# Optimization experiments

Measured on AMD Instinct MI355X. Metric: run time of the kernel, lower is better.

The kernel has to match this reference:

```python
import jax, jax.numpy as jnp
import numpy as np

C, H, R, INTER = 1024, 16, 16, 2816  # hidden, heads, lora rank, mlp intermediate
B, N = 2, 2048
EPS = 1e-5


def setup_inputs() -> dict:
    key = jax.random.key(0)
    ks = iter(jax.random.split(key, 48))
    w = lambda shape: jax.random.normal(next(ks), shape, jnp.float32) * 0.02
    d = {}
    d["x"] = jax.random.normal(next(ks), (B, N, C), jnp.float32)
    d["y"] = jax.random.normal(next(ks), (B, N, C), jnp.float32)
    d["c"] = jax.random.normal(next(ks), (B, C), jnp.float32)
    # LayerNorms
    d["gx_w"] = jnp.ones((C,)); d["gx_b"] = jnp.zeros((C,))
    d["gy_w"] = jnp.ones((C,)); d["gy_b"] = jnp.zeros((C,))
    # adaLN: SiLU -> Linear(C, 6C)
    d["ada_w"] = w((C, 6 * C)); d["ada_b"] = jnp.zeros((6 * C,))
    # two DoRA cross-attentions
    for p in ("xy", "yx"):
        d[p + "_qkv"] = w((C, 3 * C))
        d[p + "_mag"] = jnp.ones((1, H, 1, 1))
        d[p + "_la"] = w((C, R))
        d[p + "_lb"] = w((R, C))
        d[p + "_proj"] = w((C, C))
    # two HGRN recurrent attentions
    for p in ("ax", "ay"):
        d[p + "_wi"] = w((C, C))
        d[p + "_wf"] = w((C, C))
        d[p + "_wg"] = w((C, C))
        d[p + "_wo"] = w((C, C))
        d[p + "_gn"] = jnp.ones((C,))
    # two gated MLPs
    for p in ("mx", "my"):
        d[p + "_gate"] = w((C, 2 * INTER))
        d[p + "_down"] = w((INTER, C))
    return d


def _ln(v, wgt, b):
    m = v.mean(-1, keepdims=True)
    var = ((v - m) ** 2).mean(-1, keepdims=True)
    return (v - m) / jnp.sqrt(var + EPS) * wgt + b


def _modulate(v, shift, scale):
    return v * (1.0 + scale[:, None, :]) + shift[:, None, :]


def _dora_attn(q_in, Wqkv, mag, la, lb, Wp):
    # NOTE: source ignores key/value args -> self-attention on query stream
    Bq, Nq, Cq = q_in.shape
    D = Cq // H
    qkv = (q_in @ Wqkv).reshape(Bq, Nq, 3, H, D).transpose(2, 0, 3, 1, 4)
    q, k, v = qkv[0], qkv[1], qkv[2]  # [B,H,N,D]
    delta = (q_in @ la) @ lb  # LoRA delta injected into Q
    q = q + mag * delta.reshape(Bq, Nq, H, D).transpose(0, 2, 1, 3)
    attn = jax.nn.softmax(jnp.einsum('bhnd,bhmd->bhnm', q, k) * (D ** -0.5), axis=-1)
    o = jnp.einsum('bhnm,bhmd->bhnd', attn, v).transpose(0, 2, 1, 3).reshape(Bq, Nq, Cq)
    return o @ Wp


def _hgrn_attn(v, wi, wf, wg, wo, gn):
    Bv, Nv, Cv = v.shape
    D = Cv // H
    f = jax.nn.sigmoid(v @ wf)
    i = jax.nn.silu(v @ wi) * (1.0 - f)
    def step(h, ft_it):
        ft, it = ft_it
        h = ft * h + it
        return h, h
    _, hs = jax.lax.scan(step, jnp.zeros((Bv, Cv), v.dtype),
                         (f.transpose(1, 0, 2), i.transpose(1, 0, 2)))
    h = hs.transpose(1, 0, 2).reshape(Bv, Nv, H, D)
    h = h / jnp.sqrt((h * h).mean(-1, keepdims=True) + EPS)  # per-head RMSNorm
    h = (h * gn.reshape(H, D)).reshape(Bv, Nv, Cv)
    return (h * jax.nn.silu(v @ wg)) @ wo


def _mlp(v, wgate, wdown):
    u = v @ wgate
    gate, val = jnp.split(u, 2, axis=-1)
    return (jax.nn.silu(gate) * val) @ wdown


def reference(x, y, c, gx_w, gx_b, gy_w, gy_b, ada_w, ada_b,
              xy_qkv, xy_mag, xy_la, xy_lb, xy_proj,
              yx_qkv, yx_mag, yx_la, yx_lb, yx_proj,
              ax_wi, ax_wf, ax_wg, ax_wo, ax_gn,
              ay_wi, ay_wf, ay_wg, ay_wo, ay_gn,
              mx_gate, mx_down, my_gate, my_down):
    mods = jax.nn.silu(c) @ ada_w + ada_b
    sh_msa, sc_msa, g_msa, sh_mlp, sc_mlp, g_mlp = jnp.split(mods, 6, axis=1)
    x_norm = _ln(x, gx_w, gx_b)
    y_norm = _ln(y, gy_w, gy_b)
    x = x + g_msa[:, None, :] * _dora_attn(x_norm, xy_qkv, xy_mag, xy_la, xy_lb, xy_proj)
    y = y + g_msa[:, None, :] * _dora_attn(y_norm, yx_qkv, yx_mag, yx_la, yx_lb, yx_proj)
    x = x + g_msa[:, None, :] * _hgrn_attn(_modulate(x_norm, sh_msa, sc_msa), ax_wi, ax_wf, ax_wg, ax_wo, ax_gn)
    y = y + g_msa[:, None, :] * _hgrn_attn(_modulate(y_norm, sh_msa, sc_msa), ay_wi, ay_wf, ay_wg, ay_wo, ay_gn)
    x = x + g_mlp[:, None, :] * _mlp(_modulate(_ln(x, gx_w, gx_b), sh_mlp, sc_mlp), mx_gate, mx_down)
    y = y + g_mlp[:, None, :] * _mlp(_modulate(_ln(y, gy_w, gy_b), sh_mlp, sc_mlp), my_gate, my_down)
    return (x, y)
```

## Files before the change

### kernel.cpp

```cpp
#include <hip/hip_runtime.h>
#include <stdint.h>

#define NTOK 2048
#define CDIM 1024
#define ROWS 4096
#define MODS_STRIDE 6144
#define INTERDIM 2816
#define NCHUNK 32
#define CHLEN (NTOK/NCHUNK)

typedef unsigned short u16;
typedef __bf16 bf16x8 __attribute__((ext_vector_type(8)));
typedef float f32x4 __attribute__((ext_vector_type(4)));
typedef u16 u16x8 __attribute__((ext_vector_type(8)));

__device__ __forceinline__ float b2f(u16 u){
  union { unsigned int i; float f; } v; v.i = ((unsigned int)u) << 16; return v.f;
}
__device__ __forceinline__ u16 f2b(float f){
  union { float f; unsigned int i; } v; v.f = f;
  unsigned int i = v.i;
  unsigned int r = i + 0x7FFFu + ((i >> 16) & 1u);
  return (u16)(r >> 16);
}
__device__ __forceinline__ float sigm(float x){ return 1.f/(1.f+__expf(-x)); }
__device__ __forceinline__ float wredsum(float v){
#pragma unroll
  for (int o=32;o>0;o>>=1) v += __shfl_xor(v,o);
  return v;
}
__device__ __forceinline__ void async16(const void* g, void* l){
  __builtin_amdgcn_global_load_lds(
      (const __attribute__((address_space(1))) unsigned int*)g,
      (__attribute__((address_space(3))) unsigned int*)l, 16, 0, 0);
}

__global__ __launch_bounds__(256) void gemm_bt(
    const u16* __restrict__ Ain, const u16* __restrict__ Bt,
    int M, int N, int K, int epi,
    u16* __restrict__ outB,
    float* __restrict__ dest, const float* __restrict__ gate,
    float* __restrict__ outF)
{
  __shared__ u16 lA[128*32];
  __shared__ u16 lB[128*32];
  const int m0 = blockIdx.y*128, n0 = blockIdx.x*128;
  const int tid  = threadIdx.x;
  const int w    = tid>>6, lane = tid&63;
  const int quad = lane>>4, l16 = lane&15;
  const int wr = (w>>1)*64, wc = (w&1)*64;
  f32x4 acc[4][4] = {};
  const int ksteps = K >> 5;
  for (int kt=0; kt<ksteps; ++kt){
    const int k0 = kt<<5;
#pragma unroll
    for (int j=0;j<2;++j){
      const int c   = (w*2+j)*64 + lane;
      const int row = c>>2, ke = (c&3)*8;
      async16(Ain + (size_t)(m0+row)*K + k0 + ke, (char*)lA + (size_t)(w*2+j)*1024);
      async16(Bt  + (size_t)(n0+row)*K + k0 + ke, (char*)lB + (size_t)(w*2+j)*1024);
    }
    __syncthreads();
    bf16x8 af[4], bq[4];
#pragma unroll
    for (int t=0;t<4;++t){
      af[t] = *reinterpret_cast<const bf16x8*>(&lA[(wr + t*16 + l16)*32 + quad*8]);
      bq[t] = *reinterpret_cast<const bf16x8*>(&lB[(wc + t*16 + l16)*32 + quad*8]);
    }
#pragma unroll
    for (int i=0;i<4;++i)
#pragma unroll
      for (int j=0;j<4;++j)
        acc[i][j] = __builtin_amdgcn_mfma_f32_16x16x32_bf16(af[i], bq[j], acc[i][j], 0,0,0);
    __syncthreads();
  }
#pragma unroll
  for (int i=0;i<4;++i){
#pragma unroll
    for (int j=0;j<4;++j){
      const int col = n0 + wc + j*16 + l16;
#pragma unroll
      for (int r=0;r<4;++r){
        const int row = m0 + wr + i*16 + quad*4 + r;
        const float v = acc[i][j][r];
        const size_t idx = (size_t)row*N + col;
        if (epi==1){ outB[idx] = f2b(v); }
        else {
          const int b = row >> 11;
          const float v2 = dest[idx] + gate[b*MODS_STRIDE + col] * v;
          dest[idx] = v2;
          if (epi==3) outF[idx] = v2;
        }
      }
    }
  }
}

struct TDesc { const float* src; u16* dst; int rows; int cols; int base; };
struct TPack { TDesc d[16]; };

__global__ __launch_bounds__(256) void transpose_all(TPack p, int nmat)
{
  __shared__ float t[32][33];
  const int bid = blockIdx.x;
  int mi = 0;
#pragma unroll 1
  while (mi+1 < nmat && bid >= p.d[mi+1].base) ++mi;
  const TDesc D = p.d[mi];
  const int tid2   = bid - D.base;
  const int tilesx = D.cols >> 5;
  const int r0 = (tid2 / tilesx) * 32;
  const int c0 = (tid2 % tilesx) * 32;
  const int tx = threadIdx.x & 31, ty = threadIdx.x >> 5;
  for (int i=ty;i<32;i+=8)
    t[i][tx] = D.src[(size_t)(r0+i)*D.cols + c0 + tx];
  __syncthreads();
  for (int i=ty;i<32;i+=8)
    D.dst[(size_t)(c0+i)*D.rows + r0 + tx] = f2b(t[tx][i]);
}

__global__ __launch_bounds__(256) void ln_kernel(
    const float* __restrict__ xin,
    const float* __restrict__ w, const float* __restrict__ bias,
    const float* __restrict__ mods, int sh_off, int sc_off,
    u16* __restrict__ out_norm, u16* __restrict__ out_mod,
    float* __restrict__ out_xw)
{
  const int row = blockIdx.x;
  const int b = row >> 11;
  const int t = threadIdx.x;
  float v[4];
#pragma unroll
  for (int e=0;e<4;++e)
    v[e] = xin[(size_t)row*CDIM + t*4+e];
  float s  = v[0]+v[1]+v[2]+v[3];
  float ss = v[0]*v[0]+v[1]*v[1]+v[2]*v[2]+v[3]*v[3];
  s = wredsum(s); ss = wredsum(ss);
  __shared__ float rs[4], rss[4];
  const int wv = t>>6;
  if ((t&63)==0){ rs[wv]=s; rss[wv]=ss; }
  __syncthreads();
  s  = rs[0]+rs[1]+rs[2]+rs[3];
  ss = rss[0]+rss[1]+rss[2]+rss[3];
  const float mean = s * (1.f/1024.f);
  const float var  = ss * (1.f/1024.f) - mean*mean;
  const float rinv = rsqrtf(var + 1e-5f);
#pragma unroll
  for (int e=0;e<4;++e){
    const int c = t*4+e;
    const float nv = (v[e]-mean)*rinv*w[c] + bias[c];
    if (out_norm) out_norm[(size_t)row*CDIM+c] = f2b(nv);
    if (out_mod){
      const float sc = mods[b*MODS_STRIDE + sc_off + c];
      const float sh = mods[b*MODS_STRIDE + sh_off + c];
      out_mod[(size_t)row*CDIM+c] = f2b(nv*(1.f+sc)+sh);
    }
    if (out_xw) out_xw[(size_t)row*CDIM+c] = v[e];
  }
}

__global__ __launch_bounds__(256) void ada_init(
    const float* __restrict__ ab, float* __restrict__ mods)
{
  const int j = blockIdx.x*256 + threadIdx.x;
  const int jj = (j >= MODS_STRIDE) ? j - MODS_STRIDE : j;
  mods[j] = ab[jj];
}

__global__ __launch_bounds__(256) void ada_split(
    const float* __restrict__ cin, const float* __restrict__ aw,
    float* __restrict__ mods)
{
  const int j  = blockIdx.x*256 + threadIdx.x;
  const int k0 = blockIdx.y*64;
  float s0 = 0.f, s1 = 0.f;
  for (int k=k0; k<k0+64; ++k){
    const float wv = aw[(size_t)k*MODS_STRIDE + j];
    const float c0 = cin[k], c1 = cin[CDIM + k];
    s0 = fmaf(c0*sigm(c0), wv, s0);
    s1 = fmaf(c1*sigm(c1), wv, s1);
  }
  atomicAdd(&mods[j], s0);
  atomicAdd(&mods[MODS_STRIDE + j], s1);
}

__global__ __launch_bounds__(256) void lora_a(
    const u16* __restrict__ xn, const float* __restrict__ la, float* __restrict__ tmp)
{
  const int r = blockIdx.x;
  const int t = threadIdx.x;
  const int n = t & 15, slice = t >> 4;
  float s = 0.f;
  for (int kk=0;kk<64;++kk){
    const int k = slice*64 + kk;
    s = fmaf(b2f(xn[(size_t)r*CDIM + k]), la[k*16 + n], s);
  }
  __shared__ float red[256];
  red[t] = s;
  __syncthreads();
  if (t < 16){
    float tot = 0.f;
#pragma unroll
    for (int sl=0;sl<16;++sl) tot += red[sl*16 + t];
    tmp[r*16 + t] = tot;
  }
}

__global__ __launch_bounds__(256) void lora_b(
    const float* __restrict__ tmp, const float* __restrict__ lb, u16* __restrict__ delta)
{
  const unsigned int idx = blockIdx.x*256u + threadIdx.x;
  const unsigned int r = idx >> 10, c = idx & 1023u;
  float s = 0.f;
#pragma unroll
  for (int j=0;j<16;++j)
    s = fmaf(tmp[r*16 + j], lb[j*CDIM + c], s);
  delta[idx] = f2b(s);
}

__global__ __launch_bounds__(256) void attn_mfma(
    const u16* __restrict__ qkv, const u16* __restrict__ delta,
    const float* __restrict__ mag, u16* __restrict__ attn_out)
{
  __shared__ u16 Kl[64*72];
  __shared__ u16 Vt[64*72];
  __shared__ u16 Pl[4][16*72];
  const int t = threadIdx.x;
  const int w = t>>6, lane = t&63;
  const int l16 = lane&15, quad = lane>>4;
  const int qt = blockIdx.x, h = blockIdx.y, b = blockIdx.z;
  const size_t rowbase = (size_t)b*NTOK;
  const float magh = mag[h];

  bf16x8 qf[2];
  {
    const size_t gr = rowbase + qt*64 + w*16 + l16;
    const u16* qp = qkv   + gr*3072 + h*64;
    const u16* dp = delta + gr*1024 + h*64;
#pragma unroll
    for (int kw=0; kw<2; ++kw){
      const int d0 = kw*32 + quad*8;
      const u16x8 qa = *reinterpret_cast<const u16x8*>(qp + d0);
      const u16x8 da = *reinterpret_cast<const u16x8*>(dp + d0);
#pragma unroll
      for (int j=0;j<8;++j)
        qf[kw][j] = (__bf16)((b2f(qa[j]) + magh*b2f(da[j])) * 0.125f);
    }
  }

  float l_part = 0.f;
  f32x4 oacc[4] = {};

  for (int kb=0; kb<32; ++kb){
    __syncthreads();
#pragma unroll
    for (int it=0; it<2; ++it){
      const int e = it*256 + t;
      const int key = e>>3, dc = (e&7)*8;
      const u16x8 kv = *reinterpret_cast<const u16x8*>(
          qkv + (rowbase + kb*64 + key)*3072 + 1024 + h*64 + dc);
      *reinterpret_cast<u16x8*>(&Kl[key*72 + dc]) = kv;
    }
#pragma unroll
    for (int it=0; it<2; ++it){
      const int d0 = (w*2 + it)*8;
      const u16x8 vv = *reinterpret_cast<const u16x8*>(
          qkv + (rowbase + kb*64 + lane)*3072 + 2048 + h*64 + d0);
#pragma unroll
      for (int j=0;j<8;++j)
        Vt[(d0+j)*72 + lane] = vv[j];
    }
    __syncthreads();

    f32x4 sacc[4] = {};
#pragma unroll
    for (int kw=0; kw<2; ++kw){
#pragma unroll
      for (int mt=0; mt<4; ++mt){
        const bf16x8 af = *reinterpret_cast<const bf16x8*>(
            &Kl[(mt*16 + l16)*72 + kw*32 + quad*8]);
        sacc[mt] = __builtin_amdgcn_mfma_f32_16x16x32_bf16(af, qf[kw], sacc[mt], 0,0,0);
      }
    }

#pragma unroll
    for (int mt=0;mt<4;++mt)
#pragma unroll
      for (int r=0;r<4;++r){
        const float pv = __expf(sacc[mt][r]);
        sacc[mt][r] = pv;
        l_part += pv;
      }

#pragma unroll
    for (int mt=0;mt<4;++mt)
#pragma unroll
      for (int rp=0; rp<2; ++rp){
        const unsigned hi = __float_as_uint(sacc[mt][rp*2+1]);
        const unsigned lo = __float_as_uint(sacc[mt][rp*2]);
        *reinterpret_cast<unsigned*>(&Pl[w][l16*72 + mt*16 + quad*4 + rp*2]) =
            (hi & 0xFFFF0000u) | (lo >> 16);
      }

#pragma unroll
    for (int kw=0; kw<2; ++kw){
      const bf16x8 pa = *reinterpret_cast<const bf16x8*>(
          &Pl[w][l16*72 + kw*32 + quad*8]);
#pragma unroll
      for (int dt=0; dt<4; ++dt){
        const bf16x8 vb = *reinterpret_cast<const bf16x8*>(
            &Vt[(dt*16 + l16)*72 + kw*32 + quad*8]);
        oacc[dt] = __builtin_amdgcn_mfma_f32_16x16x32_bf16(pa, vb, oacc[dt], 0,0,0);
      }
    }
  }

  float l_run = l_part;
  l_run += __shfl_xor(l_run, 16);
  l_run += __shfl_xor(l_run, 32);

  float li4[4];
#pragma unroll
  for (int r=0;r<4;++r) li4[r] = __shfl(l_run, quad*4+r);
#pragma unroll
  for (int r=0;r<4;++r){
    const size_t grow = rowbase + qt*64 + w*16 + quad*4 + r;
#pragma unroll
    for (int dt=0; dt<4; ++dt)
      attn_out[grow*CDIM + h*64 + dt*16 + l16] = f2b(oacc[dt][r] / li4[r]);
  }
}

__global__ __launch_bounds__(256) void scan_p1(
    const u16* __restrict__ FIG, float* __restrict__ cA, float* __restrict__ cH)
{
  const unsigned int idx = blockIdx.x*256u + threadIdx.x;
  const unsigned int c = idx & 1023u, chunk = (idx>>10)&(NCHUNK-1), b = idx>>15;
  float A = 1.f, h = 0.f;
  const size_t base = ((size_t)b*NTOK + chunk*CHLEN) * 3072;
  for (int t=0;t<CHLEN;++t){
    const float F = b2f(FIG[base + (size_t)t*3072 + c]);
    const float I = b2f(FIG[base + (size_t)t*3072 + 1024 + c]);
    const float f = sigm(F);
    const float il = I*sigm(I) * (1.f - f);
    A *= f;
    h = fmaf(f, h, il);
  }
  cA[idx] = A; cH[idx] = h;
}

__global__ __launch_bounds__(256) void scan_p2(
    const float* __restrict__ cA, const float* __restrict__ cH, float* __restrict__ Hinit)
{
  const unsigned int idx = blockIdx.x*256u + threadIdx.x;
  const unsigned int b = idx>>10, c = idx&1023u;
  float h = 0.f;
#pragma unroll
  for (int ch=0;ch<NCHUNK;++ch){
    const unsigned int q = (b*NCHUNK + ch)*1024 + c;
    Hinit[q] = h;
    h = fmaf(cA[q], h, cH[q]);
  }
}

__global__ __launch_bounds__(256) void scan_p3(
    const u16* __restrict__ FIG, const float* __restrict__ Hinit, u16* __restrict__ Hb)
{
  const unsigned int idx = blockIdx.x*256u + threadIdx.x;
  const unsigned int c = idx & 1023u, chunk = (idx>>10)&(NCHUNK-1), b = idx>>15;
  float h = Hinit[idx];
  const size_t base = ((size_t)b*NTOK + chunk*CHLEN) * 3072;
  const size_t obase = ((size_t)b*NTOK + chunk*CHLEN) * CDIM;
  for (int t=0;t<CHLEN;++t){
    const float F = b2f(FIG[base + (size_t)t*3072 + c]);
    const float I = b2f(FIG[base + (size_t)t*3072 + 1024 + c]);
    const float f = sigm(F);
    const float il = I*sigm(I) * (1.f - f);
    h = fmaf(f, h, il);
    Hb[obase + (size_t)t*CDIM + c] = f2b(h);
  }
}

__global__ __launch_bounds__(256) void hgrn_post(
    const u16* __restrict__ Hb, const u16* __restrict__ FIG,
    const float* __restrict__ gn, u16* __restrict__ m_in)
{
  const int row = blockIdx.x;
  const int t = threadIdx.x;
  float hv[4]; float ss = 0.f;
#pragma unroll
  for (int e=0;e<4;++e){
    hv[e] = b2f(Hb[(size_t)row*CDIM + t*4 + e]);
    ss = fmaf(hv[e], hv[e], ss);
  }
#pragma unroll
  for (int o=1;o<16;o<<=1) ss += __shfl_xor(ss, o);
  const float rinv = rsqrtf(ss*(1.f/64.f) + 1e-5f);
#pragma unroll
  for (int e=0;e<4;++e){
    const int c = t*4+e;
    const float g = b2f(FIG[(size_t)row*3072 + 2048 + c]);
    m_in[(size_t)row*CDIM + c] = f2b(hv[e]*rinv*gn[c] * g*sigm(g));
  }
}

__global__ __launch_bounds__(256) void act_kernel(
    const u16* __restrict__ U, u16* __restrict__ A)
{
  const unsigned int i = blockIdx.x*256u + threadIdx.x;
  const unsigned int r = i / INTERDIM, j = i % INTERDIM;
  const float g = b2f(U[(size_t)r*(2*INTERDIM) + j]);
  const float v = b2f(U[(size_t)r*(2*INTERDIM) + INTERDIM + j]);
  A[i] = f2b(g*sigm(g)*v);
}

__global__ __launch_bounds__(256) void fill_fail(float* __restrict__ out)
{
  const unsigned int i = blockIdx.x*256u + threadIdx.x;
  out[i] = 1234.5f;
}

static void run_stream(hipStream_t stream,
    const float* Xin, const float* LNW, const float* LNB,
    const float* MAG, const float* LA, const float* LBw, const float* GN,
    float* mods, float* xw, float* outp,
    const u16* WqkvT, const u16* WprojT, const u16* WhgrnT, const u16* WwoT,
    const u16* WgateT, const u16* WdownT,
    u16* x_norm, u16* v_h, u16* qkvb, float* tmp, u16* delta, u16* attn_o,
    float* cA, float* cH, float* Hinit, u16* U, u16* actb)
{
  u16* FIG    = qkvb;
  u16* Hb     = delta;
  u16* m_in   = v_h;
  u16* mlp_in = x_norm;

  ln_kernel<<<ROWS,256,0,stream>>>(Xin, LNW, LNB, mods, 0, 1024, x_norm, v_h, xw);

  gemm_bt<<<dim3(24,32),256,0,stream>>>(x_norm, WqkvT, ROWS,3072,1024, 1, qkvb, nullptr, nullptr, nullptr);
  lora_a<<<ROWS,256,0,stream>>>(x_norm, LA, tmp);
  lora_b<<<ROWS*CDIM/256,256,0,stream>>>(tmp, LBw, delta);
  attn_mfma<<<dim3(32,16,2),256,0,stream>>>(qkvb, delta, MAG, attn_o);
  gemm_bt<<<dim3(8,32),256,0,stream>>>(attn_o, WprojT, ROWS,1024,1024, 2, nullptr, xw, mods+2048, nullptr);

  gemm_bt<<<dim3(24,32),256,0,stream>>>(v_h, WhgrnT, ROWS,3072,1024, 1, FIG, nullptr, nullptr, nullptr);
  scan_p1<<<2*NCHUNK*1024/256,256,0,stream>>>(FIG, cA, cH);
  scan_p2<<<8,256,0,stream>>>(cA, cH, Hinit);
  scan_p3<<<2*NCHUNK*1024/256,256,0,stream>>>(FIG, Hinit, Hb);
  hgrn_post<<<ROWS,256,0,stream>>>(Hb, FIG, GN, m_in);
  gemm_bt<<<dim3(8,32),256,0,stream>>>(m_in, WwoT, ROWS,1024,1024, 2, nullptr, xw, mods+2048, nullptr);

  ln_kernel<<<ROWS,256,0,stream>>>(xw, LNW, LNB, mods, 3072, 4096, nullptr, mlp_in, nullptr);
  gemm_bt<<<dim3(44,32),256,0,stream>>>(mlp_in, WgateT, ROWS,5632,1024, 1, U, nullptr, nullptr, nullptr);
  act_kernel<<<ROWS*INTERDIM/256,256,0,stream>>>(U, actb);
  gemm_bt<<<dim3(8,32),256,0,stream>>>(actb, WdownT, ROWS,1024,2816, 3, nullptr, xw, mods+5120, outp);
}

extern "C" void kernel_launch(void* const* d_in, const int* in_sizes, int n_in,
                              void* d_out, int out_size, void* d_ws, size_t ws_size,
                              hipStream_t stream)
{
  const float* X    = (const float*)d_in[0];
  const float* Y    = (const float*)d_in[1];
  const float* Cc   = (const float*)d_in[2];
  const float* GXW  = (const float*)d_in[3];
  const float* GXB  = (const float*)d_in[4];
  const float* GYW  = (const float*)d_in[5];
  const float* GYB  = (const float*)d_in[6];
  const float* ADAW = (const float*)d_in[7];
  const float* ADAB = (const float*)d_in[8];
  const float* XY_QKV = (const float*)d_in[9];
  const float* XY_MAG = (const float*)d_in[10];
  const float* XY_LA  = (const float*)d_in[11];
  const float* XY_LB  = (const float*)d_in[12];
  const float* XY_PROJ= (const float*)d_in[13];
  const float* YX_QKV = (const float*)d_in[14];
  const float* YX_MAG = (const float*)d_in[15];
  const float* YX_LA  = (const float*)d_in[16];
  const float* YX_LB  = (const float*)d_in[17];
  const float* YX_PROJ= (const float*)d_in[18];
  const float* AX_WI = (const float*)d_in[19];
  const float* AX_WF = (const float*)d_in[20];
  const float* AX_WG = (const float*)d_in[21];
  const float* AX_WO = (const float*)d_in[22];
  const float* AX_GN = (const float*)d_in[23];
  const float* AY_WI = (const float*)d_in[24];
  const float* AY_WF = (const float*)d_in[25];
  const float* AY_WG = (const float*)d_in[26];
  const float* AY_WO = (const float*)d_in[27];
  const float* AY_GN = (const float*)d_in[28];
  const float* MX_GATE = (const float*)d_in[29];
  const float* MX_DOWN = (const float*)d_in[30];
  const float* MY_GATE = (const float*)d_in[31];
  const float* MY_DOWN = (const float*)d_in[32];
  float* OUT = (float*)d_out;

  char* p = (char*)d_ws;
  size_t off = 0;
  auto alloc = [&](size_t bytes)->char*{
    char* r = p + off;
    off = (off + bytes + 255) & ~(size_t)255;
    return r;
  };
  float* mods  = (float*)alloc(2*MODS_STRIDE*sizeof(float));
  float* xw_x  = (float*)alloc((size_t)ROWS*CDIM*sizeof(float));
  float* xw_y  = (float*)alloc((size_t)ROWS*CDIM*sizeof(float));
  u16* WqkvT0  = (u16*)alloc((size_t)3072*1024*2);
  u16* WqkvT1  = (u16*)alloc((size_t)3072*1024*2);
  u16* WprojT0 = (u16*)alloc((size_t)1024*1024*2);
  u16* WprojT1 = (u16*)alloc((size_t)1024*1024*2);
  u16* WhgrnT0 = (u16*)alloc((size_t)3072*1024*2);
  u16* WhgrnT1 = (u16*)alloc((size_t)3072*1024*2);
  u16* WwoT0   = (u16*)alloc((size_t)1024*1024*2);
  u16* WwoT1   = (u16*)alloc((size_t)1024*1024*2);
  u16* WgateT0 = (u16*)alloc((size_t)5632*1024*2);
  u16* WgateT1 = (u16*)alloc((size_t)5632*1024*2);
  u16* WdownT0 = (u16*)alloc((size_t)1024*2816*2);
  u16* WdownT1 = (u16*)alloc((size_t)1024*2816*2);
  u16* x_norm  = (u16*)alloc((size_t)ROWS*CDIM*2);
  u16* v_h     = (u16*)alloc((size_t)ROWS*CDIM*2);
  u16* qkvb    = (u16*)alloc((size_t)ROWS*3072*2);
  float* tmp   = (float*)alloc((size_t)ROWS*16*sizeof(float));
  u16* delta   = (u16*)alloc((size_t)ROWS*CDIM*2);
  u16* attn_o  = (u16*)alloc((size_t)ROWS*CDIM*2);
  float* cA    = (float*)alloc((size_t)2*NCHUNK*1024*sizeof(float));
  float* cH    = (float*)alloc((size_t)2*NCHUNK*1024*sizeof(float));
  float* Hinit = (float*)alloc((size_t)2*NCHUNK*1024*sizeof(float));
  u16* U       = (u16*)alloc((size_t)ROWS*5632*2);
  u16* actb    = (u16*)alloc((size_t)ROWS*INTERDIM*2);

  if (off > ws_size){
    fill_fail<<<(2*ROWS*CDIM)/256,256,0,stream>>>(OUT);
    return;
  }

  ada_init<<<2*MODS_STRIDE/256,256,0,stream>>>(ADAB, mods);
  ada_split<<<dim3(MODS_STRIDE/256,16),256,0,stream>>>(Cc, ADAW, mods);

  TPack tp; int base = 0; int ndesc = 0;
  auto add = [&](const float* s, u16* d2, int rows, int cols){
    tp.d[ndesc].src = s; tp.d[ndesc].dst = d2;
    tp.d[ndesc].rows = rows; tp.d[ndesc].cols = cols; tp.d[ndesc].base = base;
    base += (rows>>5)*(cols>>5); ++ndesc;
  };
  add(XY_QKV,  WqkvT0, 1024, 3072);
  add(XY_PROJ, WprojT0,1024, 1024);
  add(AX_WF, WhgrnT0,               1024, 1024);
  add(AX_WI, WhgrnT0 + 1024*1024,   1024, 1024);
  add(AX_WG, WhgrnT0 + 2*1024*1024, 1024, 1024);
  add(AX_WO, WwoT0, 1024, 1024);
  add(MX_GATE, WgateT0, 1024, 5632);
  add(MX_DOWN, WdownT0, 2816, 1024);
  add(YX_QKV,  WqkvT1, 1024, 3072);
  add(YX_PROJ, WprojT1,1024, 1024);
  add(AY_WF, WhgrnT1,               1024, 1024);
  add(AY_WI, WhgrnT1 + 1024*1024,   1024, 1024);
  add(AY_WG, WhgrnT1 + 2*1024*1024, 1024, 1024);
  add(AY_WO, WwoT1, 1024, 1024);
  add(MY_GATE, WgateT1, 1024, 5632);
  add(MY_DOWN, WdownT1, 2816, 1024);
  transpose_all<<<base,256,0,stream>>>(tp, ndesc);

  run_stream(stream, X, GXW, GXB, XY_MAG, XY_LA, XY_LB, AX_GN,
             mods, xw_x, OUT,
             WqkvT0, WprojT0, WhgrnT0, WwoT0, WgateT0, WdownT0,
             x_norm, v_h, qkvb, tmp, delta, attn_o,
             cA, cH, Hinit, U, actb);

  run_stream(stream, Y, GYW, GYB, YX_MAG, YX_LA, YX_LB, AY_GN,
             mods, xw_y, OUT + (size_t)ROWS*CDIM,
             WqkvT1, WprojT1, WhgrnT1, WwoT1, WgateT1, WdownT1,
             x_norm, v_h, qkvb, tmp, delta, attn_o,
             cA, cH, Hinit, U, actb);
}
```

Before: 1.390 ms.

## Fuse proj and wo GEMMs via concatenated K and add split-K with atomics

The attention output and the HGRN output now go into one [rows,2048] buffer, and the proj and wo weights are transposed into one concatenated [1024,2048] matrix. The two residual GEMMs thereby become a single GEMM over K=2048. That GEMM and the down-projection GEMM use split-K along grid z (2 and 4 ways), with the epilogue switched to atomicAdd of gate*value into the fp32 residual. The output is then copied out by a separate kernel. The aim is to cut launches and raise the block count for the N=1024 GEMMs, which have only 256 tiles. The cost is fp32 atomic traffic, nondeterministic summation order, and an extra full copy pass.

```diff
diff --git a/kernel.cpp b/kernel.cpp
--- a/kernel.cpp
+++ b/kernel.cpp
@@ -39,20 +39,21 @@
     const u16* __restrict__ Ain, const u16* __restrict__ Bt,
     int M, int N, int K, int epi,
     u16* __restrict__ outB,
-    float* __restrict__ dest, const float* __restrict__ gate,
-    float* __restrict__ outF)
+    float* __restrict__ dest, const float* __restrict__ gate)
 {
   __shared__ u16 lA[128*32];
   __shared__ u16 lB[128*32];
   const int m0 = blockIdx.y*128, n0 = blockIdx.x*128;
+  const int kchunk = K / gridDim.z;
+  const int kbase  = blockIdx.z * kchunk;
   const int tid  = threadIdx.x;
   const int w    = tid>>6, lane = tid&63;
   const int quad = lane>>4, l16 = lane&15;
   const int wr = (w>>1)*64, wc = (w&1)*64;
   f32x4 acc[4][4] = {};
-  const int ksteps = K >> 5;
+  const int ksteps = kchunk >> 5;
   for (int kt=0; kt<ksteps; ++kt){
-    const int k0 = kt<<5;
+    const int k0 = kbase + (kt<<5);
 #pragma unroll
     for (int j=0;j<2;++j){
       const int c   = (w*2+j)*64 + lane;
@@ -87,16 +88,14 @@
         if (epi==1){ outB[idx] = f2b(v); }
         else {
           const int b = row >> 11;
-          const float v2 = dest[idx] + gate[b*MODS_STRIDE + col] * v;
-          dest[idx] = v2;
-          if (epi==3) outF[idx] = v2;
+          atomicAdd(&dest[idx], gate[b*MODS_STRIDE + col] * v);
         }
       }
     }
   }
 }
 
-struct TDesc { const float* src; u16* dst; int rows; int cols; int base; };
+struct TDesc { const float* src; u16* dst; int rows; int cols; int base; int dstride; int doff; };
 struct TPack { TDesc d[16]; };
 
 __global__ __launch_bounds__(256) void transpose_all(TPack p, int nmat)
@@ -116,7 +115,7 @@
     t[i][tx] = D.src[(size_t)(r0+i)*D.cols + c0 + tx];
   __syncthreads();
   for (int i=ty;i<32;i+=8)
-    D.dst[(size_t)(c0+i)*D.rows + r0 + tx] = f2b(t[tx][i]);
+    D.dst[(size_t)(c0+i)*D.dstride + D.doff + r0 + tx] = f2b(t[tx][i]);
 }
 
 __global__ __launch_bounds__(256) void ln_kernel(
@@ -220,7 +219,7 @@
 
 __global__ __launch_bounds__(256) void attn_mfma(
     const u16* __restrict__ qkv, const u16* __restrict__ delta,
-    const float* __restrict__ mag, u16* __restrict__ attn_out)
+    const float* __restrict__ mag, u16* __restrict__ AH)
 {
   __shared__ u16 Kl[64*72];
   __shared__ u16 Vt[64*72];
@@ -327,7 +326,7 @@
     const size_t grow = rowbase + qt*64 + w*16 + quad*4 + r;
 #pragma unroll
     for (int dt=0; dt<4; ++dt)
-      attn_out[grow*CDIM + h*64 + dt*16 + l16] = f2b(oacc[dt][r] / li4[r]);
+      AH[grow*2048 + h*64 + dt*16 + l16] = f2b(oacc[dt][r] / li4[r]);
   }
 }
 
@@ -383,7 +382,7 @@
 
 __global__ __launch_bounds__(256) void hgrn_post(
     const u16* __restrict__ Hb, const u16* __restrict__ FIG,
-    const float* __restrict__ gn, u16* __restrict__ m_in)
+    const float* __restrict__ gn, u16* __restrict__ AH)
 {
   const int row = blockIdx.x;
   const int t = threadIdx.x;
@@ -400,7 +399,7 @@
   for (int e=0;e<4;++e){
     const int c = t*4+e;
     const float g = b2f(FIG[(size_t)row*3072 + 2048 + c]);
-    m_in[(size_t)row*CDIM + c] = f2b(hv[e]*rinv*gn[c] * g*sigm(g));
+    AH[(size_t)row*2048 + 1024 + c] = f2b(hv[e]*rinv*gn[c] * g*sigm(g));
   }
 }
 
@@ -414,6 +413,13 @@
   A[i] = f2b(g*sigm(g)*v);
 }
 
+__global__ __launch_bounds__(256) void store_out(
+    const float* __restrict__ xw, float* __restrict__ out)
+{
+  const unsigned int i = blockIdx.x*256u + threadIdx.x;
+  out[i] = xw[i];
+}
+
 __global__ __launch_bounds__(256) void fill_fail(float* __restrict__ out)
 {
   const unsigned int i = blockIdx.x*256u + threadIdx.x;
@@ -424,35 +430,36 @@
     const float* Xin, const float* LNW, const float* LNB,
     const float* MAG, const float* LA, const float* LBw, const float* GN,
     float* mods, float* xw, float* outp,
-    const u16* WqkvT, const u16* WprojT, const u16* WhgrnT, const u16* WwoT,
+    const u16* WqkvT, const u16* WpwT, const u16* WhgrnT,
     const u16* WgateT, const u16* WdownT,
-    u16* x_norm, u16* v_h, u16* qkvb, float* tmp, u16* delta, u16* attn_o,
+    u16* x_norm, u16* v_h, u16* qkvb, float* tmp, u16* delta, u16* AH,
     float* cA, float* cH, float* Hinit, u16* U, u16* actb)
 {
   u16* FIG    = qkvb;
   u16* Hb     = delta;
-  u16* m_in   = v_h;
   u16* mlp_in = x_norm;
 
   ln_kernel<<<ROWS,256,0,stream>>>(Xin, LNW, LNB, mods, 0, 1024, x_norm, v_h, xw);
 
-  gemm_bt<<<dim3(24,32),256,0,stream>>>(x_norm, WqkvT, ROWS,3072,1024, 1, qkvb, nullptr, nullptr, nullptr);
+  gemm_bt<<<dim3(24,32),256,0,stream>>>(x_norm, WqkvT, ROWS,3072,1024, 1, qkvb, nullptr, nullptr);
   lora_a<<<ROWS,256,0,stream>>>(x_norm, LA, tmp);
   lora_b<<<ROWS*CDIM/256,256,0,stream>>>(tmp, LBw, delta);
-  attn_mfma<<<dim3(32,16,2),256,0,stream>>>(qkvb, delta, MAG, attn_o);
-  gemm_bt<<<dim3(8,32),256,0,stream>>>(attn_o, WprojT, ROWS,1024,1024, 2, nullptr, xw, mods+2048, nullptr);
-
-  gemm_bt<<<dim3(24,32),256,0,stream>>>(v_h, WhgrnT, ROWS,3072,1024, 1, FIG, nullptr, nullptr, nullptr);
+  attn_mfma<<<dim3(32,16,2),256,0,stream>>>(qkvb, delta, MAG, AH);
+
+  gemm_bt<<<dim3(24,32),256,0,stream>>>(v_h, WhgrnT, ROWS,3072,1024, 1, FIG, nullptr, nullptr);
   scan_p1<<<2*NCHUNK*1024/256,256,0,stream>>>(FIG, cA, cH);
   scan_p2<<<8,256,0,stream>>>(cA, cH, Hinit);
   scan_p3<<<2*NCHUNK*1024/256,256,0,stream>>>(FIG, Hinit, Hb);
-  hgrn_post<<<ROWS,256,0,stream>>>(Hb, FIG, GN, m_in);
-  gemm_bt<<<dim3(8,32),256,0,stream>>>(m_in, WwoT, ROWS,1024,1024, 2, nullptr, xw, mods+2048, nullptr);
+  hgrn_post<<<ROWS,256,0,stream>>>(Hb, FIG, GN, AH);
+
+  gemm_bt<<<dim3(8,32,2),256,0,stream>>>(AH, WpwT, ROWS,1024,2048, 2, nullptr, xw, mods+2048);
 
   ln_kernel<<<ROWS,256,0,stream>>>(xw, LNW, LNB, mods, 3072, 4096, nullptr, mlp_in, nullptr);
-  gemm_bt<<<dim3(44,32),256,0,stream>>>(mlp_in, WgateT, ROWS,5632,1024, 1, U, nullptr, nullptr, nullptr);
+  gemm_bt<<<dim3(44,32),256,0,stream>>>(mlp_in, WgateT, ROWS,5632,1024, 1, U, nullptr, nullptr);
   act_kernel<<<ROWS*INTERDIM/256,256,0,stream>>>(U, actb);
-  gemm_bt<<<dim3(8,32),256,0,stream>>>(actb, WdownT, ROWS,1024,2816, 3, nullptr, xw, mods+5120, outp);
+  gemm_bt<<<dim3(8,32,4),256,0,stream>>>(actb, WdownT, ROWS,1024,2816, 2, nullptr, xw, mods+5120);
+
+  store_out<<<ROWS*CDIM/256,256,0,stream>>>(xw, outp);
 }
 
 extern "C" void kernel_launch(void* const* d_in, const int* in_sizes, int n_in,
@@ -506,12 +513,10 @@
   float* xw_y  = (float*)alloc((size_t)ROWS*CDIM*sizeof(float));
   u16* WqkvT0  = (u16*)alloc((size_t)3072*1024*2);
   u16* WqkvT1  = (u16*)alloc((size_t)3072*1024*2);
-  u16* WprojT0 = (u16*)alloc((size_t)1024*1024*2);
-  u16* WprojT1 = (u16*)alloc((size_t)1024*1024*2);
+  u16* WpwT0   = (u16*)alloc((size_t)1024*2048*2);
+  u16* WpwT1   = (u16*)alloc((size_t)1024*2048*2);
   u16* WhgrnT0 = (u16*)alloc((size_t)3072*1024*2);
   u16* WhgrnT1 = (u16*)alloc((size_t)3072*1024*2);
-  u16* WwoT0   = (u16*)alloc((size_t)1024*1024*2);
-  u16* WwoT1   = (u16*)alloc((size_t)1024*1024*2);
   u16* WgateT0 = (u16*)alloc((size_t)5632*1024*2);
   u16* WgateT1 = (u16*)alloc((size_t)5632*1024*2);
   u16* WdownT0 = (u16*)alloc((size_t)1024*2816*2);
@@ -521,7 +526,7 @@
   u16* qkvb    = (u16*)alloc((size_t)ROWS*3072*2);
   float* tmp   = (float*)alloc((size_t)ROWS*16*sizeof(float));
   u16* delta   = (u16*)alloc((size_t)ROWS*CDIM*2);
-  u16* attn_o  = (u16*)alloc((size_t)ROWS*CDIM*2);
+  u16* AH      = (u16*)alloc((size_t)ROWS*2048*2);
   float* cA    = (float*)alloc((size_t)2*NCHUNK*1024*sizeof(float));
   float* cH    = (float*)alloc((size_t)2*NCHUNK*1024*sizeof(float));
   float* Hinit = (float*)alloc((size_t)2*NCHUNK*1024*sizeof(float));
@@ -537,38 +542,39 @@
   ada_split<<<dim3(MODS_STRIDE/256,16),256,0,stream>>>(Cc, ADAW, mods);
 
   TPack tp; int base = 0; int ndesc = 0;
-  auto add = [&](const float* s, u16* d2, int rows, int cols){
+  auto add = [&](const float* s, u16* d2, int rows, int cols, int dstride, int doff){
     tp.d[ndesc].src = s; tp.d[ndesc].dst = d2;
     tp.d[ndesc].rows = rows; tp.d[ndesc].cols = cols; tp.d[ndesc].base = base;
+    tp.d[ndesc].dstride = dstride; tp.d[ndesc].doff = doff;
     base += (rows>>5)*(cols>>5); ++ndesc;
   };
-  add(XY_QKV,  WqkvT0, 1024, 3072);
-  add(XY_PROJ, WprojT0,1024, 1024);
-  add(AX_WF, WhgrnT0,               1024, 1024);
-  add(AX_WI, WhgrnT0 + 1024*1024,   1024, 1024);
-  add(AX_WG, WhgrnT0 + 2*1024*1024, 1024, 1024);
-  add(AX_WO, WwoT0, 1024, 1024);
-  add(MX_GATE, WgateT0, 1024, 5632);
-  add(MX_DOWN, WdownT0, 2816, 1024);
-  add(YX_QKV,  WqkvT1, 1024, 3072);
-  add(YX_PROJ, WprojT1,1024, 1024);
-  add(AY_WF, WhgrnT1,               1024, 1024);
-  add(AY_WI, WhgrnT1 + 1024*1024,   1024, 1024);
-  add(AY_WG, WhgrnT1 + 2*1024*1024, 1024, 1024);
-  add(AY_WO, WwoT1, 1024, 1024);
-  add(MY_GATE, WgateT1, 1024, 5632);
-  add(MY_DOWN, WdownT1, 2816, 1024);
+  add(XY_QKV,  WqkvT0, 1024, 3072, 1024, 0);
+  add(XY_PROJ, WpwT0,  1024, 1024, 2048, 0);
+  add(AX_WO,   WpwT0,  1024, 1024, 2048, 1024);
+  add(AX_WF, WhgrnT0,               1024, 1024, 1024, 0);
+  add(AX_WI, WhgrnT0 + 1024*1024,   1024, 1024, 1024, 0);
+  add(AX_WG, WhgrnT0 + 2*1024*1024, 1024, 1024, 1024, 0);
+  add(MX_GATE, WgateT0, 1024, 5632, 1024, 0);
+  add(MX_DOWN, WdownT0, 2816, 1024, 2816, 0);
+  add(YX_QKV,  WqkvT1, 1024, 3072, 1024, 0);
+  add(YX_PROJ, WpwT1,  1024, 1024, 2048, 0);
+  add(AY_WO,   WpwT1,  1024, 1024, 2048, 1024);
+  add(AY_WF, WhgrnT1,               1024, 1024, 1024, 0);
+  add(AY_WI, WhgrnT1 + 1024*1024,   1024, 1024, 1024, 0);
+  add(AY_WG, WhgrnT1 + 2*1024*1024, 1024, 1024, 1024, 0);
+  add(MY_GATE, WgateT1, 1024, 5632, 1024, 0);
+  add(MY_DOWN, WdownT1, 2816, 1024, 2816, 0);
   transpose_all<<<base,256,0,stream>>>(tp, ndesc);
 
   run_stream(stream, X, GXW, GXB, XY_MAG, XY_LA, XY_LB, AX_GN,
              mods, xw_x, OUT,
-             WqkvT0, WprojT0, WhgrnT0, WwoT0, WgateT0, WdownT0,
-             x_norm, v_h, qkvb, tmp, delta, attn_o,
+             WqkvT0, WpwT0, WhgrnT0, WgateT0, WdownT0,
+             x_norm, v_h, qkvb, tmp, delta, AH,
              cA, cH, Hinit, U, actb);
 
   run_stream(stream, Y, GYW, GYB, YX_MAG, YX_LA, YX_LB, AY_GN,
              mods, xw_y, OUT + (size_t)ROWS*CDIM,
-             WqkvT1, WprojT1, WhgrnT1, WwoT1, WgateT1, WdownT1,
-             x_norm, v_h, qkvb, tmp, delta, attn_o,
+             WqkvT1, WpwT1, WhgrnT1, WgateT1, WdownT1,
+             x_norm, v_h, qkvb, tmp, delta, AH,
              cA, cH, Hinit, U, actb);
 }
```

Measured after the change: 1.388 ms. About the same (-0.2%).
